# Performance work log

Hardware: AMD Instinct MI355X
Metric: run time of the kernel (lower is better)

Reference implementation:

```python
import jax, jax.numpy as jnp
import numpy as np

TOP_K = 2
LN_EPS = 1e-5
GATE_EPS = 1e-6


def setup_inputs() -> dict:
    key = jax.random.key(0)
    ks = jax.random.split(key, 5)
    B, D, E, H, O = 16384, 1200, 8, 1024, 1
    x = jax.random.normal(ks[0], (B, D), dtype=jnp.float32)
    w_gate = jax.random.normal(ks[1], (D, E), dtype=jnp.float32) * 0.05
    W1 = jax.random.normal(ks[2], (E, D, H), dtype=jnp.float32) * (1.0 / np.sqrt(D))
    b1 = jnp.zeros((E, H), dtype=jnp.float32)
    g1 = jnp.ones((E, H), dtype=jnp.float32)   # LayerNorm weight
    be1 = jnp.zeros((E, H), dtype=jnp.float32)  # LayerNorm bias
    W2 = jax.random.normal(ks[3], (E, H, O), dtype=jnp.float32) * (1.0 / np.sqrt(H))
    b2 = jnp.zeros((E, O), dtype=jnp.float32)
    return {"x": x, "w_gate": w_gate, "W1": W1, "b1": b1, "g1": g1, "be1": be1, "W2": W2, "b2": b2}


def reference(x, w_gate, W1, b1, g1, be1, W2, b2):
    B = x.shape[0]
    # --- top-k gating (eval mode: no noise) ---
    probs = jax.nn.softmax(x @ w_gate, axis=1)                 # [B, E]
    top_vals, top_idx = jax.lax.top_k(probs, TOP_K)            # [B, k]
    top_gates = top_vals / (jnp.sum(top_vals, axis=1, keepdims=True) + GATE_EPS)
    gates = jnp.zeros_like(probs).at[jnp.arange(B)[:, None], top_idx].set(top_gates)  # [B, E]
    # --- per-expert MLP (computed densely for all experts; gates zero out non-selected) ---
    h = jnp.einsum('bd,edh->beh', x, W1) + b1                  # [B, E, H]
    mu = jnp.mean(h, axis=-1, keepdims=True)
    var = jnp.var(h, axis=-1, keepdims=True)
    h = (h - mu) * jax.lax.rsqrt(var + LN_EPS) * g1 + be1      # LayerNorm
    h = jax.nn.relu(h)
    out = jax.nn.sigmoid(jnp.einsum('beh,eho->beo', h, W2) + b2)  # [B, E, O]
    # --- scatter/combine: weighted sum over experts ---
    y = jnp.einsum('be,beo->bo', gates, out)                   # [B, O]
    return y
```

## Files before the change

### kernel.cpp

```cpp
#include <hip/hip_runtime.h>
#include <hip/hip_bf16.h>
#include <stdint.h>

#define B_ROWS 16384
#define D_IN   1200
#define D_PAD  1216
#define N_EXP  8
#define H_DIM  1024
#define CAP    33792
#define N_TILES 264
#define LN_EPS 1e-5f
#define GATE_EPS 1e-6f
#define CNT_STRIDE 16

#define O_CNT    0
#define O_POFF   512
#define O_CNT2   576
#define O_TOPI   1088
#define O_TOPG   132160
#define O_PROWC  263232
#define O_PGATEC 398400
#define O_XBF    533568
#define O_W1T    40381888
#define O_HBUF   60304832

#define GATING_BLOCKS (B_ROWS / 32)
#define W1T_BLOCKS    (19 * 16 * 8)

typedef short bf16x8 __attribute__((ext_vector_type(8)));
typedef short short8 __attribute__((ext_vector_type(8)));
typedef short short4v __attribute__((ext_vector_type(4)));
typedef float f32x4 __attribute__((ext_vector_type(4)));

__device__ __forceinline__ void load_lds16(const void* gptr, void* ldsptr) {
    __builtin_amdgcn_global_load_lds(
        (__attribute__((address_space(1))) void*)const_cast<void*>(gptr),
        (__attribute__((address_space(3))) void*)ldsptr, 16, 0, 0);
}

__device__ __forceinline__ short4v pack_bf16x4(float4 a) {
    union { short4v v; __hip_bfloat16 h[4]; } u;
    u.h[0] = __float2bfloat16(a.x); u.h[1] = __float2bfloat16(a.y);
    u.h[2] = __float2bfloat16(a.z); u.h[3] = __float2bfloat16(a.w);
    return u.v;
}

__global__ __launch_bounds__(256) void gating_w1t_kernel(
    const float* __restrict__ x, const float* __restrict__ wg,
    const float* __restrict__ W1,
    int* __restrict__ topIdx, float* __restrict__ topGate,
    int* __restrict__ cnt,
    __hip_bfloat16* __restrict__ w1t, __hip_bfloat16* __restrict__ xbf)
{
    __shared__ float tile[2][32][33];
    __shared__ int lhist[N_EXP];
    int bx = blockIdx.x;
    int tid = threadIdx.x;

    if (bx < GATING_BLOCKS) {
        if (tid < N_EXP) lhist[tid] = 0;
        __syncthreads();

        int widx = tid >> 6;
        int lane = tid & 63;
        int rowbase = bx * 32 + widx * 8;
        const float* xw = x + (long)rowbase * D_IN;

        float acc[8][8];
#pragma unroll
        for (int r = 0; r < 8; ++r)
#pragma unroll
            for (int e = 0; e < N_EXP; ++e) acc[r][e] = 0.f;

        for (int i = lane; i < 304; i += 64) {
            if (i < 300) {
                const float4* wv4 = (const float4*)(wg + (long)i * 32);
                float4 w0 = wv4[0], w1v = wv4[1], w2 = wv4[2], w3 = wv4[3],
                       w4 = wv4[4], w5 = wv4[5], w6 = wv4[6], w7 = wv4[7];
#pragma unroll
                for (int r = 0; r < 8; ++r) {
                    float4 xv = ((const float4*)(xw + (long)r * D_IN))[i];
                    acc[r][0] += xv.x * w0.x + xv.y * w2.x + xv.z * w4.x + xv.w * w6.x;
                    acc[r][1] += xv.x * w0.y + xv.y * w2.y + xv.z * w4.y + xv.w * w6.y;
                    acc[r][2] += xv.x * w0.z + xv.y * w2.z + xv.z * w4.z + xv.w * w6.z;
                    acc[r][3] += xv.x * w0.w + xv.y * w2.w + xv.z * w4.w + xv.w * w6.w;
                    acc[r][4] += xv.x * w1v.x + xv.y * w3.x + xv.z * w5.x + xv.w * w7.x;
                    acc[r][5] += xv.x * w1v.y + xv.y * w3.y + xv.z * w5.y + xv.w * w7.y;
                    acc[r][6] += xv.x * w1v.z + xv.y * w3.z + xv.z * w5.z + xv.w * w7.z;
                    acc[r][7] += xv.x * w1v.w + xv.y * w3.w + xv.z * w5.w + xv.w * w7.w;
                    ((short4v*)(xbf + (long)(rowbase + r) * D_PAD))[i] = pack_bf16x4(xv);
                }
            } else {
#pragma unroll
                for (int r = 0; r < 8; ++r)
                    ((short4v*)(xbf + (long)(rowbase + r) * D_PAD))[i] = (short4v){0, 0, 0, 0};
            }
        }

#pragma unroll
        for (int r = 0; r < 8; ++r)
#pragma unroll
            for (int e = 0; e < N_EXP; ++e) {
                float v = acc[r][e];
#pragma unroll
                for (int off = 32; off > 0; off >>= 1) v += __shfl_xor(v, off, 64);
                acc[r][e] = v;
            }

        float my[N_EXP];
#pragma unroll
        for (int e = 0; e < N_EXP; ++e) my[e] = acc[0][e];
#pragma unroll
        for (int r = 1; r < 8; ++r)
#pragma unroll
            for (int e = 0; e < N_EXP; ++e)
                if (lane == r) my[e] = acc[r][e];

        if (lane < 8) {
            float m = my[0];
#pragma unroll
            for (int e = 1; e < N_EXP; ++e) m = fmaxf(m, my[e]);
            float p[N_EXP], s = 0.f;
#pragma unroll
            for (int e = 0; e < N_EXP; ++e) { p[e] = expf(my[e] - m); s += p[e]; }
            int i0 = 0;
#pragma unroll
            for (int e = 1; e < N_EXP; ++e) if (p[e] > p[i0]) i0 = e;
            int i1 = (i0 == 0) ? 1 : 0;
#pragma unroll
            for (int e = 0; e < N_EXP; ++e) if (e != i0 && p[e] > p[i1]) i1 = e;
            float v0 = p[i0] / s, v1 = p[i1] / s;
            float inv = 1.f / (v0 + v1 + GATE_EPS);
            int row = rowbase + lane;
            ((int2*)topIdx)[row] = make_int2(i0, i1);
            ((float2*)topGate)[row] = make_float2(v0 * inv, v1 * inv);
            atomicAdd(&lhist[i0], 1);
            atomicAdd(&lhist[i1], 1);
        }
        __syncthreads();
        if (tid < N_EXP) atomicAdd(&cnt[tid * CNT_STRIDE], lhist[tid]);
    } else if (bx == GATING_BLOCKS) {
        short8* xrow = (short8*)(xbf + (long)B_ROWS * D_PAD);
        if (tid < 152) xrow[tid] = (short8){0, 0, 0, 0, 0, 0, 0, 0};
    } else {
        int b = bx - GATING_BLOCKS - 1;
        int d0 = (b % 19) * 64;
        int h0 = ((b / 19) % 16) * 64;
        int e = b / (19 * 16);
        const float* src = W1 + (long)e * D_IN * H_DIM;

        int hs = tid & 15;
        int dr = tid >> 4;
#pragma unroll
        for (int s = 0; s < 4; ++s) {
            int dl = dr + 16 * s;
            int d = d0 + dl;
            float4 v = (d < D_IN)
                ? ((const float4*)(src + (long)d * H_DIM + h0))[hs]
                : (float4){0.f, 0.f, 0.f, 0.f};
            int drl = dl & 31;
            int hl = hs * 4;
            int Th = hl >> 5;
            int hh = hl & 31;
            tile[Th][drl][hh + 0] = v.x;
            tile[Th][drl][hh + 1] = v.y;
            tile[Th][drl][hh + 2] = v.z;
            tile[Th][drl][hh + 3] = v.w;
            if (s == 1) {
                __syncthreads();
                int T2 = tid >> 7, rr = tid & 127;
                int hl2 = rr >> 2, dseg = rr & 3;
                float f[8];
#pragma unroll
                for (int j = 0; j < 8; ++j) f[j] = tile[T2][dseg * 8 + j][hl2];
                union { short8 v8; __hip_bfloat16 hh8[8]; } u;
#pragma unroll
                for (int j = 0; j < 8; ++j) u.hh8[j] = __float2bfloat16(f[j]);
                int h = h0 + T2 * 32 + hl2;
                ((short8*)(w1t + (long)e * H_DIM * D_PAD + (long)h * D_PAD + d0))[dseg] = u.v8;
                __syncthreads();
            }
        }
        __syncthreads();
        {
            int T2 = tid >> 7, rr = tid & 127;
            int hl2 = rr >> 2, dseg = rr & 3;
            float f[8];
#pragma unroll
            for (int j = 0; j < 8; ++j) f[j] = tile[T2][dseg * 8 + j][hl2];
            union { short8 v8; __hip_bfloat16 hh8[8]; } u;
#pragma unroll
            for (int j = 0; j < 8; ++j) u.hh8[j] = __float2bfloat16(f[j]);
            int h = h0 + T2 * 32 + hl2;
            ((short8*)(w1t + (long)e * H_DIM * D_PAD + (long)h * D_PAD + d0 + 32))[dseg] = u.v8;
        }
    }
}

__global__ void offsets_kernel(const int* __restrict__ cnt, int* __restrict__ poff)
{
    if (threadIdx.x == 0 && blockIdx.x == 0) {
        int o = 0;
        for (int e = 0; e < N_EXP; ++e) {
            poff[e] = o;
            o += (cnt[e * CNT_STRIDE] + 127) & ~127;
        }
        poff[N_EXP] = o;
    }
}

__global__ __launch_bounds__(256) void scatter_kernel(
    const int* __restrict__ topIdx, const float* __restrict__ topGate,
    const int* __restrict__ cnt, const int* __restrict__ poff, int* __restrict__ cnt2,
    int* __restrict__ pairRowC, float* __restrict__ pairGateC, float* __restrict__ y)
{
    int tid = threadIdx.x;
    int b = blockIdx.x;

    {
        int p = b * 256 + tid;
        int e = 0;
        while (e < N_EXP - 1 && p >= poff[e + 1]) ++e;
        if (p - poff[e] >= cnt[e * CNT_STRIDE]) {
            pairRowC[p] = B_ROWS;
            pairGateC[p] = 0.f;
        }
    }
    if (b >= B_ROWS / 256) return;

    int row = b * 256 + tid;
    y[row] = 0.f;

    __shared__ int lcnt[N_EXP];
    __shared__ int base[N_EXP];
    if (tid < N_EXP) lcnt[tid] = 0;
    __syncthreads();
    int2 e = ((const int2*)topIdx)[row];
    float2 g = ((const float2*)topGate)[row];
    int s0 = atomicAdd(&lcnt[e.x], 1);
    int s1 = atomicAdd(&lcnt[e.y], 1);
    __syncthreads();
    if (tid < N_EXP) base[tid] = atomicAdd(&cnt2[tid * CNT_STRIDE], lcnt[tid]);
    __syncthreads();
    int p0 = poff[e.x] + base[e.x] + s0;
    pairRowC[p0] = row; pairGateC[p0] = g.x;
    int p1 = poff[e.y] + base[e.y] + s1;
    pairRowC[p1] = row; pairGateC[p1] = g.y;
}

__global__ __launch_bounds__(256) void gemm_kernel(
    const __hip_bfloat16* __restrict__ xbf, const __hip_bfloat16* __restrict__ w1t,
    const float* __restrict__ b1, const int* __restrict__ poff,
    const int* __restrict__ pairRowC,
    __hip_bfloat16* __restrict__ hbuf)
{
    int bi = blockIdx.x;
    int xcd = bi & 7;
    int j = bi >> 3;
    int col0 = (j & 7) << 7;
    int rt = xcd * 33 + (j >> 3);
    int row0 = rt << 7;
    if (row0 >= poff[N_EXP]) return;
    int e = 0;
    while (e < N_EXP - 1 && row0 >= poff[e + 1]) ++e;

    __shared__ short lA[2][128 * 32];
    __shared__ short lB[2][128 * 32];

    int t = threadIdx.x;
    int lane = t & 63, w = t >> 6;
    int wm = (w >> 1) * 64, wn = (w & 1) * 64;
    int l15 = lane & 15, quad = lane >> 4;
    int qsw = quad ^ ((l15 >> 1) & 3);

    f32x4 acc[4][4];
#pragma unroll
    for (int i = 0; i < 4; ++i)
#pragma unroll
        for (int j2 = 0; j2 < 4; ++j2) acc[i][j2] = (f32x4){0.f, 0.f, 0.f, 0.f};

    int r1 = t >> 2, seg = t & 3;
    int sw = seg ^ ((r1 >> 1) & 3);
    int ridx1 = pairRowC[row0 + r1];
    int ridx2 = pairRowC[row0 + 64 + r1];
    const __hip_bfloat16* Arow1 = xbf + (long)ridx1 * D_PAD + sw * 8;
    const __hip_bfloat16* Arow2 = xbf + (long)ridx2 * D_PAD + sw * 8;
    const __hip_bfloat16* Bb = w1t + (long)e * H_DIM * D_PAD + (long)col0 * D_PAD;
    const __hip_bfloat16* Brow1 = Bb + (long)r1 * D_PAD + sw * 8;
    const __hip_bfloat16* Brow2 = Bb + (long)(r1 + 64) * D_PAD + sw * 8;

    for (int kt = 0; kt < D_PAD / 64; ++kt) {
        __syncthreads();
        int k0 = kt * 64;
        load_lds16(Arow1 + k0,      (char*)lA[0] + t * 16);
        load_lds16(Arow2 + k0,      (char*)lA[0] + t * 16 + 4096);
        load_lds16(Arow1 + k0 + 32, (char*)lA[1] + t * 16);
        load_lds16(Arow2 + k0 + 32, (char*)lA[1] + t * 16 + 4096);
        load_lds16(Brow1 + k0,      (char*)lB[0] + t * 16);
        load_lds16(Brow2 + k0,      (char*)lB[0] + t * 16 + 4096);
        load_lds16(Brow1 + k0 + 32, (char*)lB[1] + t * 16);
        load_lds16(Brow2 + k0 + 32, (char*)lB[1] + t * 16 + 4096);
        __syncthreads();

#pragma unroll
        for (int p = 0; p < 2; ++p) {
            const char* lAc = (const char*)lA[p];
            const char* lBc = (const char*)lB[p];
            bf16x8 af[4], bfr[4];
#pragma unroll
            for (int i = 0; i < 4; ++i)
                af[i] = *(const bf16x8*)(lAc + (wm + i * 16 + l15) * 64 + qsw * 16);
#pragma unroll
            for (int j2 = 0; j2 < 4; ++j2)
                bfr[j2] = *(const bf16x8*)(lBc + (wn + j2 * 16 + l15) * 64 + qsw * 16);
#pragma unroll
            for (int i = 0; i < 4; ++i)
#pragma unroll
                for (int j2 = 0; j2 < 4; ++j2)
                    acc[i][j2] = __builtin_amdgcn_mfma_f32_16x16x32_bf16(af[i], bfr[j2], acc[i][j2], 0, 0, 0);
        }
    }

#pragma unroll
    for (int i = 0; i < 4; ++i) {
        int lr = wm + i * 16 + quad * 4;
#pragma unroll
        for (int j2 = 0; j2 < 4; ++j2) {
            int gc = col0 + wn + j2 * 16 + l15;
            float bias = b1[e * H_DIM + gc];
#pragma unroll
            for (int r = 0; r < 4; ++r) {
                float v = acc[i][j2][r] + bias;
                hbuf[(long)(row0 + lr + r) * H_DIM + gc] = __float2bfloat16(v);
            }
        }
    }
}

__global__ __launch_bounds__(256) void ln_head_kernel(
    const __hip_bfloat16* __restrict__ hbuf, const int* __restrict__ cnt, const int* __restrict__ poff,
    const int* __restrict__ pairRowC, const float* __restrict__ pairGateC,
    const float* __restrict__ g1, const float* __restrict__ be1,
    const float* __restrict__ W2, const float* __restrict__ b2,
    float* __restrict__ y)
{
    int tid = threadIdx.x;
    int p = blockIdx.x * 4 + (tid >> 6);
    if (p >= poff[N_EXP]) return;
    int e = 0;
    while (e < N_EXP - 1 && p >= poff[e + 1]) ++e;
    if (p - poff[e] >= cnt[e * CNT_STRIDE]) return;

    int lane = tid & 63;
    int row = pairRowC[p];
    float gate = pairGateC[p];
    const short4v* hr = (const short4v*)(hbuf + (long)p * H_DIM);

    float v[16];
    float sum = 0.f, sumsq = 0.f;
#pragma unroll
    for (int k = 0; k < 4; ++k) {
        union { short4v s; __hip_bfloat16 h[4]; } hv;
        hv.s = hr[lane + k * 64];
#pragma unroll
        for (int j = 0; j < 4; ++j) {
            float f = __bfloat162float(hv.h[j]);
            v[k * 4 + j] = f;
            sum += f;
            sumsq += f * f;
        }
    }
#pragma unroll
    for (int off = 32; off > 0; off >>= 1) {
        sum += __shfl_xor(sum, off, 64);
        sumsq += __shfl_xor(sumsq, off, 64);
    }
    float mu = sum * (1.f / H_DIM);
    float var = sumsq * (1.f / H_DIM) - mu * mu;
    float rstd = rsqrtf(var + LN_EPS);

    float z = 0.f;
#pragma unroll
    for (int k = 0; k < 4; ++k) {
        float4 gv = ((const float4*)(g1 + e * H_DIM))[lane + k * 64];
        float4 bv = ((const float4*)(be1 + e * H_DIM))[lane + k * 64];
        float4 wv = ((const float4*)(W2 + e * H_DIM))[lane + k * 64];
        z += fmaxf((v[k*4+0] - mu) * rstd * gv.x + bv.x, 0.f) * wv.x;
        z += fmaxf((v[k*4+1] - mu) * rstd * gv.y + bv.y, 0.f) * wv.y;
        z += fmaxf((v[k*4+2] - mu) * rstd * gv.z + bv.z, 0.f) * wv.z;
        z += fmaxf((v[k*4+3] - mu) * rstd * gv.w + bv.w, 0.f) * wv.w;
    }
#pragma unroll
    for (int off = 32; off > 0; off >>= 1) z += __shfl_xor(z, off, 64);
    if (lane == 0) {
        float zt = z + b2[e];
        float o = 1.f / (1.f + expf(-zt));
        atomicAdd(&y[row], gate * o);
    }
}

extern "C" void kernel_launch(void* const* d_in, const int* in_sizes, int n_in,
                              void* d_out, int out_size, void* d_ws, size_t ws_size,
                              hipStream_t stream)
{
    const float* x   = (const float*)d_in[0];
    const float* wg  = (const float*)d_in[1];
    const float* W1  = (const float*)d_in[2];
    const float* b1  = (const float*)d_in[3];
    const float* g1  = (const float*)d_in[4];
    const float* be1 = (const float*)d_in[5];
    const float* W2  = (const float*)d_in[6];
    const float* b2  = (const float*)d_in[7];
    float* y = (float*)d_out;

    char* ws = (char*)d_ws;
    int*   cnt       = (int*)(ws + O_CNT);
    int*   poff      = (int*)(ws + O_POFF);
    int*   cnt2      = (int*)(ws + O_CNT2);
    int*   topIdx    = (int*)(ws + O_TOPI);
    float* topGate   = (float*)(ws + O_TOPG);
    int*   pairRowC  = (int*)(ws + O_PROWC);
    float* pairGateC = (float*)(ws + O_PGATEC);
    __hip_bfloat16* xbf  = (__hip_bfloat16*)(ws + O_XBF);
    __hip_bfloat16* w1t  = (__hip_bfloat16*)(ws + O_W1T);
    __hip_bfloat16* hbuf = (__hip_bfloat16*)(ws + O_HBUF);

    hipMemsetAsync(ws, 0, 1088, stream);

    gating_w1t_kernel<<<GATING_BLOCKS + 1 + W1T_BLOCKS, 256, 0, stream>>>(
        x, wg, W1, topIdx, topGate, cnt, w1t, xbf);
    offsets_kernel<<<1, 64, 0, stream>>>(cnt, poff);
    scatter_kernel<<<CAP / 256, 256, 0, stream>>>(topIdx, topGate, cnt, poff, cnt2,
                                                  pairRowC, pairGateC, y);
    gemm_kernel<<<N_TILES * 8, 256, 0, stream>>>(xbf, w1t, b1, poff, pairRowC, hbuf);
    ln_head_kernel<<<(CAP + 3) / 4, 256, 0, stream>>>(hbuf, cnt, poff, pairRowC, pairGateC,
                                                      g1, be1, W2, b2, y);
}
```

Before: 315.3 us.

## Split gating/W1 transpose kernels, inline offsets, halve GEMM K-step

Splits the fused gating-plus-W1-transpose kernel into two separate launches. The single-thread offsets kernel is removed; each consumer kernel now computes the per-expert padded offsets from the counts itself. The GEMM K-tile shrinks from 64 to 32 per barrier pair, halving LDS usage but doubling the number of barriers and load phases. The kernel split gives up the concurrency the fused launch had between gating and the transpose, and the smaller K-step lowers the MFMA work per synchronisation.

```diff
diff --git a/kernel.cpp b/kernel.cpp
--- a/kernel.cpp
+++ b/kernel.cpp
@@ -14,7 +14,6 @@
 #define CNT_STRIDE 16
 
 #define O_CNT    0
-#define O_POFF   512
 #define O_CNT2   576
 #define O_TOPI   1088
 #define O_TOPG   132160
@@ -45,144 +44,141 @@
     return u.v;
 }
 
-__global__ __launch_bounds__(256) void gating_w1t_kernel(
+__device__ __forceinline__ void load_poff(const int* __restrict__ cnt, int* pf) {
+    pf[0] = 0;
+#pragma unroll
+    for (int q = 0; q < N_EXP; ++q)
+        pf[q + 1] = pf[q] + ((cnt[q * CNT_STRIDE] + 127) & ~127);
+}
+
+__global__ __launch_bounds__(256) void gating_kernel(
     const float* __restrict__ x, const float* __restrict__ wg,
-    const float* __restrict__ W1,
     int* __restrict__ topIdx, float* __restrict__ topGate,
-    int* __restrict__ cnt,
-    __hip_bfloat16* __restrict__ w1t, __hip_bfloat16* __restrict__ xbf)
-{
-    __shared__ float tile[2][32][33];
+    int* __restrict__ cnt, __hip_bfloat16* __restrict__ xbf)
+{
     __shared__ int lhist[N_EXP];
     int bx = blockIdx.x;
     int tid = threadIdx.x;
 
-    if (bx < GATING_BLOCKS) {
-        if (tid < N_EXP) lhist[tid] = 0;
-        __syncthreads();
-
-        int widx = tid >> 6;
-        int lane = tid & 63;
-        int rowbase = bx * 32 + widx * 8;
-        const float* xw = x + (long)rowbase * D_IN;
-
-        float acc[8][8];
-#pragma unroll
-        for (int r = 0; r < 8; ++r)
-#pragma unroll
-            for (int e = 0; e < N_EXP; ++e) acc[r][e] = 0.f;
-
-        for (int i = lane; i < 304; i += 64) {
-            if (i < 300) {
-                const float4* wv4 = (const float4*)(wg + (long)i * 32);
-                float4 w0 = wv4[0], w1v = wv4[1], w2 = wv4[2], w3 = wv4[3],
-                       w4 = wv4[4], w5 = wv4[5], w6 = wv4[6], w7 = wv4[7];
-#pragma unroll
-                for (int r = 0; r < 8; ++r) {
-                    float4 xv = ((const float4*)(xw + (long)r * D_IN))[i];
-                    acc[r][0] += xv.x * w0.x + xv.y * w2.x + xv.z * w4.x + xv.w * w6.x;
-                    acc[r][1] += xv.x * w0.y + xv.y * w2.y + xv.z * w4.y + xv.w * w6.y;
-                    acc[r][2] += xv.x * w0.z + xv.y * w2.z + xv.z * w4.z + xv.w * w6.z;
-                    acc[r][3] += xv.x * w0.w + xv.y * w2.w + xv.z * w4.w + xv.w * w6.w;
-                    acc[r][4] += xv.x * w1v.x + xv.y * w3.x + xv.z * w5.x + xv.w * w7.x;
-                    acc[r][5] += xv.x * w1v.y + xv.y * w3.y + xv.z * w5.y + xv.w * w7.y;
-                    acc[r][6] += xv.x * w1v.z + xv.y * w3.z + xv.z * w5.z + xv.w * w7.z;
-                    acc[r][7] += xv.x * w1v.w + xv.y * w3.w + xv.z * w5.w + xv.w * w7.w;
-                    ((short4v*)(xbf + (long)(rowbase + r) * D_PAD))[i] = pack_bf16x4(xv);
-                }
-            } else {
-#pragma unroll
-                for (int r = 0; r < 8; ++r)
-                    ((short4v*)(xbf + (long)(rowbase + r) * D_PAD))[i] = (short4v){0, 0, 0, 0};
-            }
-        }
-
-#pragma unroll
-        for (int r = 0; r < 8; ++r)
-#pragma unroll
-            for (int e = 0; e < N_EXP; ++e) {
-                float v = acc[r][e];
-#pragma unroll
-                for (int off = 32; off > 0; off >>= 1) v += __shfl_xor(v, off, 64);
-                acc[r][e] = v;
-            }
-
-        float my[N_EXP];
-#pragma unroll
-        for (int e = 0; e < N_EXP; ++e) my[e] = acc[0][e];
-#pragma unroll
-        for (int r = 1; r < 8; ++r)
-#pragma unroll
-            for (int e = 0; e < N_EXP; ++e)
-                if (lane == r) my[e] = acc[r][e];
-
-        if (lane < 8) {
-            float m = my[0];
-#pragma unroll
-            for (int e = 1; e < N_EXP; ++e) m = fmaxf(m, my[e]);
-            float p[N_EXP], s = 0.f;
-#pragma unroll
-            for (int e = 0; e < N_EXP; ++e) { p[e] = expf(my[e] - m); s += p[e]; }
-            int i0 = 0;
-#pragma unroll
-            for (int e = 1; e < N_EXP; ++e) if (p[e] > p[i0]) i0 = e;
-            int i1 = (i0 == 0) ? 1 : 0;
-#pragma unroll
-            for (int e = 0; e < N_EXP; ++e) if (e != i0 && p[e] > p[i1]) i1 = e;
-            float v0 = p[i0] / s, v1 = p[i1] / s;
-            float inv = 1.f / (v0 + v1 + GATE_EPS);
-            int row = rowbase + lane;
-            ((int2*)topIdx)[row] = make_int2(i0, i1);
-            ((float2*)topGate)[row] = make_float2(v0 * inv, v1 * inv);
-            atomicAdd(&lhist[i0], 1);
-            atomicAdd(&lhist[i1], 1);
-        }
-        __syncthreads();
-        if (tid < N_EXP) atomicAdd(&cnt[tid * CNT_STRIDE], lhist[tid]);
-    } else if (bx == GATING_BLOCKS) {
+    if (bx == GATING_BLOCKS) {
         short8* xrow = (short8*)(xbf + (long)B_ROWS * D_PAD);
         if (tid < 152) xrow[tid] = (short8){0, 0, 0, 0, 0, 0, 0, 0};
-    } else {
-        int b = bx - GATING_BLOCKS - 1;
-        int d0 = (b % 19) * 64;
-        int h0 = ((b / 19) % 16) * 64;
-        int e = b / (19 * 16);
-        const float* src = W1 + (long)e * D_IN * H_DIM;
-
-        int hs = tid & 15;
-        int dr = tid >> 4;
-#pragma unroll
-        for (int s = 0; s < 4; ++s) {
-            int dl = dr + 16 * s;
-            int d = d0 + dl;
-            float4 v = (d < D_IN)
-                ? ((const float4*)(src + (long)d * H_DIM + h0))[hs]
-                : (float4){0.f, 0.f, 0.f, 0.f};
-            int drl = dl & 31;
-            int hl = hs * 4;
-            int Th = hl >> 5;
-            int hh = hl & 31;
-            tile[Th][drl][hh + 0] = v.x;
-            tile[Th][drl][hh + 1] = v.y;
-            tile[Th][drl][hh + 2] = v.z;
-            tile[Th][drl][hh + 3] = v.w;
-            if (s == 1) {
-                __syncthreads();
-                int T2 = tid >> 7, rr = tid & 127;
-                int hl2 = rr >> 2, dseg = rr & 3;
-                float f[8];
-#pragma unroll
-                for (int j = 0; j < 8; ++j) f[j] = tile[T2][dseg * 8 + j][hl2];
-                union { short8 v8; __hip_bfloat16 hh8[8]; } u;
-#pragma unroll
-                for (int j = 0; j < 8; ++j) u.hh8[j] = __float2bfloat16(f[j]);
-                int h = h0 + T2 * 32 + hl2;
-                ((short8*)(w1t + (long)e * H_DIM * D_PAD + (long)h * D_PAD + d0))[dseg] = u.v8;
-                __syncthreads();
+        return;
+    }
+
+    if (tid < N_EXP) lhist[tid] = 0;
+    __syncthreads();
+
+    int widx = tid >> 6;
+    int lane = tid & 63;
+    int rowbase = bx * 32 + widx * 8;
+    const float* xw = x + (long)rowbase * D_IN;
+
+    float acc[8][8];
+#pragma unroll
+    for (int r = 0; r < 8; ++r)
+#pragma unroll
+        for (int e = 0; e < N_EXP; ++e) acc[r][e] = 0.f;
+
+    for (int i = lane; i < 304; i += 64) {
+        if (i < 300) {
+            const float4* wv4 = (const float4*)(wg + (long)i * 32);
+            float4 w0 = wv4[0], w1v = wv4[1], w2 = wv4[2], w3 = wv4[3],
+                   w4 = wv4[4], w5 = wv4[5], w6 = wv4[6], w7 = wv4[7];
+#pragma unroll
+            for (int r = 0; r < 8; ++r) {
+                float4 xv = ((const float4*)(xw + (long)r * D_IN))[i];
+                acc[r][0] += xv.x * w0.x + xv.y * w2.x + xv.z * w4.x + xv.w * w6.x;
+                acc[r][1] += xv.x * w0.y + xv.y * w2.y + xv.z * w4.y + xv.w * w6.y;
+                acc[r][2] += xv.x * w0.z + xv.y * w2.z + xv.z * w4.z + xv.w * w6.z;
+                acc[r][3] += xv.x * w0.w + xv.y * w2.w + xv.z * w4.w + xv.w * w6.w;
+                acc[r][4] += xv.x * w1v.x + xv.y * w3.x + xv.z * w5.x + xv.w * w7.x;
+                acc[r][5] += xv.x * w1v.y + xv.y * w3.y + xv.z * w5.y + xv.w * w7.y;
+                acc[r][6] += xv.x * w1v.z + xv.y * w3.z + xv.z * w5.z + xv.w * w7.z;
+                acc[r][7] += xv.x * w1v.w + xv.y * w3.w + xv.z * w5.w + xv.w * w7.w;
+                ((short4v*)(xbf + (long)(rowbase + r) * D_PAD))[i] = pack_bf16x4(xv);
             }
-        }
-        __syncthreads();
-        {
+        } else {
+#pragma unroll
+            for (int r = 0; r < 8; ++r)
+                ((short4v*)(xbf + (long)(rowbase + r) * D_PAD))[i] = (short4v){0, 0, 0, 0};
+        }
+    }
+
+#pragma unroll
+    for (int r = 0; r < 8; ++r)
+#pragma unroll
+        for (int e = 0; e < N_EXP; ++e) {
+            float v = acc[r][e];
+#pragma unroll
+            for (int off = 32; off > 0; off >>= 1) v += __shfl_xor(v, off, 64);
+            acc[r][e] = v;
+        }
+
+    float my[N_EXP];
+#pragma unroll
+    for (int e = 0; e < N_EXP; ++e) my[e] = acc[0][e];
+#pragma unroll
+    for (int r = 1; r < 8; ++r)
+#pragma unroll
+        for (int e = 0; e < N_EXP; ++e)
+            if (lane == r) my[e] = acc[r][e];
+
+    if (lane < 8) {
+        float m = my[0];
+#pragma unroll
+        for (int e = 1; e < N_EXP; ++e) m = fmaxf(m, my[e]);
+        float p[N_EXP], s = 0.f;
+#pragma unroll
+        for (int e = 0; e < N_EXP; ++e) { p[e] = expf(my[e] - m); s += p[e]; }
+        int i0 = 0;
+#pragma unroll
+        for (int e = 1; e < N_EXP; ++e) if (p[e] > p[i0]) i0 = e;
+        int i1 = (i0 == 0) ? 1 : 0;
+#pragma unroll
+        for (int e = 0; e < N_EXP; ++e) if (e != i0 && p[e] > p[i1]) i1 = e;
+        float v0 = p[i0] / s, v1 = p[i1] / s;
+        float inv = 1.f / (v0 + v1 + GATE_EPS);
+        int row = rowbase + lane;
+        ((int2*)topIdx)[row] = make_int2(i0, i1);
+        ((float2*)topGate)[row] = make_float2(v0 * inv, v1 * inv);
+        atomicAdd(&lhist[i0], 1);
+        atomicAdd(&lhist[i1], 1);
+    }
+    __syncthreads();
+    if (tid < N_EXP) atomicAdd(&cnt[tid * CNT_STRIDE], lhist[tid]);
+}
+
+__global__ __launch_bounds__(256) void w1t_kernel(
+    const float* __restrict__ W1, __hip_bfloat16* __restrict__ w1t)
+{
+    __shared__ float tile[2][32][33];
+    int b = blockIdx.x;
+    int tid = threadIdx.x;
+    int d0 = (b % 19) * 64;
+    int h0 = ((b / 19) % 16) * 64;
+    int e = b / (19 * 16);
+    const float* src = W1 + (long)e * D_IN * H_DIM;
+
+    int hs = tid & 15;
+    int dr = tid >> 4;
+#pragma unroll
+    for (int s = 0; s < 4; ++s) {
+        int dl = dr + 16 * s;
+        int d = d0 + dl;
+        float4 v = (d < D_IN)
+            ? ((const float4*)(src + (long)d * H_DIM + h0))[hs]
+            : (float4){0.f, 0.f, 0.f, 0.f};
+        int drl = dl & 31;
+        int hl = hs * 4;
+        int Th = hl >> 5;
+        int hh = hl & 31;
+        tile[Th][drl][hh + 0] = v.x;
+        tile[Th][drl][hh + 1] = v.y;
+        tile[Th][drl][hh + 2] = v.z;
+        tile[Th][drl][hh + 3] = v.w;
+        if (s == 1) {
+            __syncthreads();
             int T2 = tid >> 7, rr = tid & 127;
             int hl2 = rr >> 2, dseg = rr & 3;
             float f[8];
@@ -192,36 +188,40 @@
 #pragma unroll
             for (int j = 0; j < 8; ++j) u.hh8[j] = __float2bfloat16(f[j]);
             int h = h0 + T2 * 32 + hl2;
-            ((short8*)(w1t + (long)e * H_DIM * D_PAD + (long)h * D_PAD + d0 + 32))[dseg] = u.v8;
-        }
-    }
-}
-
-__global__ void offsets_kernel(const int* __restrict__ cnt, int* __restrict__ poff)
-{
-    if (threadIdx.x == 0 && blockIdx.x == 0) {
-        int o = 0;
-        for (int e = 0; e < N_EXP; ++e) {
-            poff[e] = o;
-            o += (cnt[e * CNT_STRIDE] + 127) & ~127;
-        }
-        poff[N_EXP] = o;
+            ((short8*)(w1t + (long)e * H_DIM * D_PAD + (long)h * D_PAD + d0))[dseg] = u.v8;
+            __syncthreads();
+        }
+    }
+    __syncthreads();
+    {
+        int T2 = tid >> 7, rr = tid & 127;
+        int hl2 = rr >> 2, dseg = rr & 3;
+        float f[8];
+#pragma unroll
+        for (int j = 0; j < 8; ++j) f[j] = tile[T2][dseg * 8 + j][hl2];
+        union { short8 v8; __hip_bfloat16 hh8[8]; } u;
+#pragma unroll
+        for (int j = 0; j < 8; ++j) u.hh8[j] = __float2bfloat16(f[j]);
+        int h = h0 + T2 * 32 + hl2;
+        ((short8*)(w1t + (long)e * H_DIM * D_PAD + (long)h * D_PAD + d0 + 32))[dseg] = u.v8;
     }
 }
 
 __global__ __launch_bounds__(256) void scatter_kernel(
     const int* __restrict__ topIdx, const float* __restrict__ topGate,
-    const int* __restrict__ cnt, const int* __restrict__ poff, int* __restrict__ cnt2,
+    const int* __restrict__ cnt, int* __restrict__ cnt2,
     int* __restrict__ pairRowC, float* __restrict__ pairGateC, float* __restrict__ y)
 {
     int tid = threadIdx.x;
     int b = blockIdx.x;
+    int pf[N_EXP + 1];
+    load_poff(cnt, pf);
 
     {
         int p = b * 256 + tid;
         int e = 0;
-        while (e < N_EXP - 1 && p >= poff[e + 1]) ++e;
-        if (p - poff[e] >= cnt[e * CNT_STRIDE]) {
+        while (e < N_EXP - 1 && p >= pf[e + 1]) ++e;
+        if (p - pf[e] >= cnt[e * CNT_STRIDE]) {
             pairRowC[p] = B_ROWS;
             pairGateC[p] = 0.f;
         }
@@ -242,30 +242,33 @@
     __syncthreads();
     if (tid < N_EXP) base[tid] = atomicAdd(&cnt2[tid * CNT_STRIDE], lcnt[tid]);
     __syncthreads();
-    int p0 = poff[e.x] + base[e.x] + s0;
+    int p0 = pf[e.x] + base[e.x] + s0;
     pairRowC[p0] = row; pairGateC[p0] = g.x;
-    int p1 = poff[e.y] + base[e.y] + s1;
+    int p1 = pf[e.y] + base[e.y] + s1;
     pairRowC[p1] = row; pairGateC[p1] = g.y;
 }
 
 __global__ __launch_bounds__(256) void gemm_kernel(
     const __hip_bfloat16* __restrict__ xbf, const __hip_bfloat16* __restrict__ w1t,
-    const float* __restrict__ b1, const int* __restrict__ poff,
+    const float* __restrict__ b1, const int* __restrict__ cnt,
     const int* __restrict__ pairRowC,
     __hip_bfloat16* __restrict__ hbuf)
 {
+    int pf[N_EXP + 1];
+    load_poff(cnt, pf);
+
     int bi = blockIdx.x;
     int xcd = bi & 7;
     int j = bi >> 3;
     int col0 = (j & 7) << 7;
     int rt = xcd * 33 + (j >> 3);
     int row0 = rt << 7;
-    if (row0 >= poff[N_EXP]) return;
+    if (row0 >= pf[N_EXP]) return;
     int e = 0;
-    while (e < N_EXP - 1 && row0 >= poff[e + 1]) ++e;
-
-    __shared__ short lA[2][128 * 32];
-    __shared__ short lB[2][128 * 32];
+    while (e < N_EXP - 1 && row0 >= pf[e + 1]) ++e;
+
+    __shared__ short lA[128 * 32];
+    __shared__ short lB[128 * 32];
 
     int t = threadIdx.x;
     int lane = t & 63, w = t >> 6;
@@ -288,37 +291,30 @@
     const __hip_bfloat16* Bb = w1t + (long)e * H_DIM * D_PAD + (long)col0 * D_PAD;
     const __hip_bfloat16* Brow1 = Bb + (long)r1 * D_PAD + sw * 8;
     const __hip_bfloat16* Brow2 = Bb + (long)(r1 + 64) * D_PAD + sw * 8;
-
-    for (int kt = 0; kt < D_PAD / 64; ++kt) {
+    char* lAc = (char*)lA;
+    char* lBc = (char*)lB;
+
+    for (int kt = 0; kt < D_PAD / 32; ++kt) {
         __syncthreads();
-        int k0 = kt * 64;
-        load_lds16(Arow1 + k0,      (char*)lA[0] + t * 16);
-        load_lds16(Arow2 + k0,      (char*)lA[0] + t * 16 + 4096);
-        load_lds16(Arow1 + k0 + 32, (char*)lA[1] + t * 16);
-        load_lds16(Arow2 + k0 + 32, (char*)lA[1] + t * 16 + 4096);
-        load_lds16(Brow1 + k0,      (char*)lB[0] + t * 16);
-        load_lds16(Brow2 + k0,      (char*)lB[0] + t * 16 + 4096);
-        load_lds16(Brow1 + k0 + 32, (char*)lB[1] + t * 16);
-        load_lds16(Brow2 + k0 + 32, (char*)lB[1] + t * 16 + 4096);
+        int k0 = kt * 32;
+        load_lds16(Arow1 + k0, lAc + t * 16);
+        load_lds16(Arow2 + k0, lAc + t * 16 + 4096);
+        load_lds16(Brow1 + k0, lBc + t * 16);
+        load_lds16(Brow2 + k0, lBc + t * 16 + 4096);
         __syncthreads();
 
-#pragma unroll
-        for (int p = 0; p < 2; ++p) {
-            const char* lAc = (const char*)lA[p];
-            const char* lBc = (const char*)lB[p];
-            bf16x8 af[4], bfr[4];
-#pragma unroll
-            for (int i = 0; i < 4; ++i)
-                af[i] = *(const bf16x8*)(lAc + (wm + i * 16 + l15) * 64 + qsw * 16);
+        bf16x8 af[4], bfr[4];
+#pragma unroll
+        for (int i = 0; i < 4; ++i)
+            af[i] = *(const bf16x8*)(lAc + (wm + i * 16 + l15) * 64 + qsw * 16);
+#pragma unroll
+        for (int j2 = 0; j2 < 4; ++j2)
+            bfr[j2] = *(const bf16x8*)(lBc + (wn + j2 * 16 + l15) * 64 + qsw * 16);
+#pragma unroll
+        for (int i = 0; i < 4; ++i)
 #pragma unroll
             for (int j2 = 0; j2 < 4; ++j2)
-                bfr[j2] = *(const bf16x8*)(lBc + (wn + j2 * 16 + l15) * 64 + qsw * 16);
-#pragma unroll
-            for (int i = 0; i < 4; ++i)
-#pragma unroll
-                for (int j2 = 0; j2 < 4; ++j2)
-                    acc[i][j2] = __builtin_amdgcn_mfma_f32_16x16x32_bf16(af[i], bfr[j2], acc[i][j2], 0, 0, 0);
-        }
+                acc[i][j2] = __builtin_amdgcn_mfma_f32_16x16x32_bf16(af[i], bfr[j2], acc[i][j2], 0, 0, 0);
     }
 
 #pragma unroll
@@ -338,18 +334,21 @@
 }
 
 __global__ __launch_bounds__(256) void ln_head_kernel(
-    const __hip_bfloat16* __restrict__ hbuf, const int* __restrict__ cnt, const int* __restrict__ poff,
+    const __hip_bfloat16* __restrict__ hbuf, const int* __restrict__ cnt,
     const int* __restrict__ pairRowC, const float* __restrict__ pairGateC,
     const float* __restrict__ g1, const float* __restrict__ be1,
     const float* __restrict__ W2, const float* __restrict__ b2,
     float* __restrict__ y)
 {
+    int pf[N_EXP + 1];
+    load_poff(cnt, pf);
+
     int tid = threadIdx.x;
     int p = blockIdx.x * 4 + (tid >> 6);
-    if (p >= poff[N_EXP]) return;
+    if (p >= pf[N_EXP]) return;
     int e = 0;
-    while (e < N_EXP - 1 && p >= poff[e + 1]) ++e;
-    if (p - poff[e] >= cnt[e * CNT_STRIDE]) return;
+    while (e < N_EXP - 1 && p >= pf[e + 1]) ++e;
+    if (p - pf[e] >= cnt[e * CNT_STRIDE]) return;
 
     int lane = tid & 63;
     int row = pairRowC[p];
@@ -415,7 +414,6 @@
 
     char* ws = (char*)d_ws;
     int*   cnt       = (int*)(ws + O_CNT);
-    int*   poff      = (int*)(ws + O_POFF);
     int*   cnt2      = (int*)(ws + O_CNT2);
     int*   topIdx    = (int*)(ws + O_TOPI);
     float* topGate   = (float*)(ws + O_TOPG);
@@ -427,12 +425,11 @@
 
     hipMemsetAsync(ws, 0, 1088, stream);
 
-    gating_w1t_kernel<<<GATING_BLOCKS + 1 + W1T_BLOCKS, 256, 0, stream>>>(
-        x, wg, W1, topIdx, topGate, cnt, w1t, xbf);
-    offsets_kernel<<<1, 64, 0, stream>>>(cnt, poff);
-    scatter_kernel<<<CAP / 256, 256, 0, stream>>>(topIdx, topGate, cnt, poff, cnt2,
+    gating_kernel<<<GATING_BLOCKS + 1, 256, 0, stream>>>(x, wg, topIdx, topGate, cnt, xbf);
+    w1t_kernel<<<W1T_BLOCKS, 256, 0, stream>>>(W1, w1t);
+    scatter_kernel<<<CAP / 256, 256, 0, stream>>>(topIdx, topGate, cnt, cnt2,
                                                   pairRowC, pairGateC, y);
-    gemm_kernel<<<N_TILES * 8, 256, 0, stream>>>(xbf, w1t, b1, poff, pairRowC, hbuf);
-    ln_head_kernel<<<(CAP + 3) / 4, 256, 0, stream>>>(hbuf, cnt, poff, pairRowC, pairGateC,
+    gemm_kernel<<<N_TILES * 8, 256, 0, stream>>>(xbf, w1t, b1, cnt, pairRowC, hbuf);
+    ln_head_kernel<<<(CAP + 3) / 4, 256, 0, stream>>>(hbuf, cnt, pairRowC, pairGateC,
                                                       g1, be1, W2, b2, y);
 }
```

New measurement: 310.4 us. Within noise of the previous version (-1.6%).
